# Kernel tuning notes

Hardware: AMD Instinct MI355X
Metric: run time of the kernel (lower is better)

The kernel has to match this reference:

```python
import jax, jax.numpy as jnp
import numpy as np

E = 8        # num_experts
D = 512      # embed_size
H = 8        # attention heads
HD = D // H  # head dim
B, S = 4, 1024


def setup_inputs() -> dict:
    key = jax.random.key(0)
    ks = jax.random.split(key, 16)
    sd = 0.02
    return {
        "x":  jax.random.normal(ks[0], (B, S, D), jnp.float32),
        # per-expert FFN params, stacked over expert dim
        "W1": jax.random.normal(ks[1], (E, D, 4 * D), jnp.float32) * sd,
        "b1": jnp.zeros((E, 4 * D), jnp.float32),
        "W2": jax.random.normal(ks[2], (E, 4 * D, D), jnp.float32) * sd,
        "b2": jnp.zeros((E, D), jnp.float32),
        # MultiheadAttention in_proj (split) and out_proj
        "Wq": jax.random.normal(ks[3], (D, D), jnp.float32) * sd,
        "bq": jnp.zeros((D,), jnp.float32),
        "Wk": jax.random.normal(ks[4], (D, D), jnp.float32) * sd,
        "bk": jnp.zeros((D,), jnp.float32),
        "Wv": jax.random.normal(ks[5], (D, D), jnp.float32) * sd,
        "bv": jnp.zeros((D,), jnp.float32),
        "Wo": jax.random.normal(ks[6], (D, D), jnp.float32) * sd,
        "bo": jnp.zeros((D,), jnp.float32),
        "expert_id": 3,
    }


def reference(x, W1, b1, W2, b2, Wq, bq, Wk, bk, Wv, bv, Wo, bo, expert_id):
    # --- batched per-expert FFN (fuses the Python loop over experts) ---
    # hidden: [B, E, S, 4D]
    hidden = jax.nn.relu(jnp.einsum('bsd,edf->besf', x, W1) + b1[None, :, None, :])
    eo = jnp.einsum('besf,efd->besd', hidden, W2) + b2[None, :, None, :]  # [B,E,S,D]
    eo = eo.transpose(0, 2, 1, 3)  # [B, S, E, D]

    Bs, Ss = x.shape[0], x.shape[1]
    a = eo.reshape(Bs * Ss, E, D)  # [N, E, D]; attention runs over the expert dim

    # --- MultiheadAttention (batch_first), torch semantics ---
    # NOTE: the original passes a FLOAT tril-of-ones attn_mask, which torch ADDS
    # to the scores (it does NOT mask with -inf). We reproduce that faithfully.
    q = (a @ Wq.T + bq).reshape(-1, E, H, HD).transpose(0, 2, 1, 3)  # [N,H,E,hd]
    k = (a @ Wk.T + bk).reshape(-1, E, H, HD).transpose(0, 2, 1, 3)
    v = (a @ Wv.T + bv).reshape(-1, E, H, HD).transpose(0, 2, 1, 3)

    mask = jnp.tril(jnp.ones((E, E), jnp.float32))  # additive float mask
    scores = jnp.einsum('nhed,nhfd->nhef', q, k) / jnp.sqrt(jnp.float32(HD))
    scores = scores + mask[None, None, :, :]
    attn = jax.nn.softmax(scores, axis=-1)
    ctx = jnp.einsum('nhef,nhfd->nhed', attn, v)           # [N,H,E,hd]
    ctx = ctx.transpose(0, 2, 1, 3).reshape(-1, E, D)       # [N,E,D]
    out = ctx @ Wo.T + bo                                   # [N,E,D]

    out = out.reshape(Bs, Ss, E, D)
    return out[:, :, expert_id, :]  # [B, S, D]
```

## Files before the change

### kernel.cpp

```cpp
#include <hip/hip_runtime.h>
#include <hip/hip_bf16.h>

typedef __hip_bfloat16 bf16;
typedef __attribute__((ext_vector_type(4))) float f32x4;
typedef __attribute__((ext_vector_type(8))) short s16x8;

#define N_TOK 4096
#define Dm    512
#define Fm    2048
#define Em    8

__device__ __forceinline__ float bf2f(bf16 v) { return __bfloat162float(v); }
__device__ __forceinline__ bf16  f2bf(float f) { return __float2bfloat16(f); }

#define GL16(g, l)                                                              \
  __builtin_amdgcn_global_load_lds(                                             \
      (const __attribute__((address_space(1))) void*)(g),                       \
      (__attribute__((address_space(3))) void*)(l), 16, 0, 0)

#define BAR()                                   \
  do {                                          \
    __builtin_amdgcn_s_barrier();               \
    asm volatile("" ::: "memory");              \
  } while (0)

__global__ void cvt_f32_bf16(const float* __restrict__ in, bf16* __restrict__ out, int n4) {
  int i = blockIdx.x * 256 + threadIdx.x;
  if (i >= n4) return;
  float4 v = reinterpret_cast<const float4*>(in)[i];
  bf16 tmp[4] = {f2bf(v.x), f2bf(v.y), f2bf(v.z), f2bf(v.w)};
  __builtin_memcpy(out + (size_t)i * 4, tmp, 8);
}

__global__ void transpose_cvt(const float* __restrict__ in, bf16* __restrict__ out,
                              int R, int C, long inb, long outb) {
  in  += (long)blockIdx.z * inb;
  out += (long)blockIdx.z * outb;
  __shared__ float t[32][33];
  int tx = threadIdx.x & 31, ty = threadIdx.x >> 5;
  int c0 = blockIdx.x * 32, r0 = blockIdx.y * 32;
#pragma unroll
  for (int i = 0; i < 32; i += 8)
    t[ty + i][tx] = in[(long)(r0 + ty + i) * C + c0 + tx];
  __syncthreads();
#pragma unroll
  for (int i = 0; i < 32; i += 8)
    out[(long)(c0 + ty + i) * R + r0 + tx] = f2bf(t[tx][ty + i]);
}

template <bool RELU, bool OUT_BF16>
__global__ __launch_bounds__(512, 2) void gemm2b(
    const bf16* __restrict__ A, const bf16* __restrict__ Bt, void* __restrict__ Cout,
    const float* __restrict__ bias, int K, int lda, int ldb, int ldc,
    long abs_, long bbs, long cbs, long biasbs) {
  __shared__ bf16 lds[2 * 16384];

  int e  = blockIdx.z;
  int bm = blockIdx.x * 256, bn = blockIdx.y * 256;

  A    += (long)e * abs_;
  Bt   += (long)e * bbs;
  bias += (long)e * biasbs;
  long coff = (long)e * cbs;

  int tid = threadIdx.x, wv = tid >> 6, lane = tid & 63;
  int wm = wv >> 2, wn = wv & 3;
  int la = lane & 15, q = lane >> 4;

  const bf16* Ab = A + (long)bm * lda;
  const bf16* Bb = Bt + (long)bn * ldb;
  int nt = K >> 5;

  int srow = tid >> 2;
  int ls   = (tid & 3) ^ ((srow >> 1) & 3);
  long aoff0 = (long)srow * lda + ls * 8, aoff1 = aoff0 + (long)128 * lda;
  long boff0 = (long)srow * ldb + ls * 8, boff1 = boff0 + (long)128 * ldb;
  int dst0 = (wv * 64) * 8, dst1 = (512 + wv * 64) * 8;

  auto stage = [&](int t) {
    if (t >= nt) return;
    bf16* buf = lds + (t & 1) * 16384;
    int k0 = t << 5;
    GL16(Ab + aoff0 + k0, buf + dst0);
    GL16(Ab + aoff1 + k0, buf + dst1);
    GL16(Bb + boff0 + k0, buf + 8192 + dst0);
    GL16(Bb + boff1 + k0, buf + 8192 + dst1);
  };

  f32x4 acc[8][4] = {};
  s16x8 af[4], bfr[4];

  stage(0);

  for (int t = 0; t < nt; ++t) {
    asm volatile("s_waitcnt vmcnt(0)" ::: "memory");
    BAR();
    stage(t + 1);
    const bf16* Abuf = lds + (t & 1) * 16384;
    const bf16* Bbuf = Abuf + 8192;
#pragma unroll
    for (int m = 0; m < 4; ++m) {
      int r = wm * 128 + m * 16 + la;
      af[m] = *reinterpret_cast<const s16x8*>(Abuf + r * 32 + ((q ^ ((r >> 1) & 3)) * 8));
    }
#pragma unroll
    for (int n = 0; n < 4; ++n) {
      int r = wn * 64 + n * 16 + la;
      bfr[n] = *reinterpret_cast<const s16x8*>(Bbuf + r * 32 + ((q ^ ((r >> 1) & 3)) * 8));
    }
    __builtin_amdgcn_s_setprio(1);
#pragma unroll
    for (int m = 0; m < 4; ++m)
#pragma unroll
      for (int n = 0; n < 4; ++n)
        acc[m][n] = __builtin_amdgcn_mfma_f32_16x16x32_bf16(bfr[n], af[m], acc[m][n], 0, 0, 0);
    __builtin_amdgcn_s_setprio(0);
#pragma unroll
    for (int m = 0; m < 4; ++m) {
      int r = wm * 128 + 64 + m * 16 + la;
      af[m] = *reinterpret_cast<const s16x8*>(Abuf + r * 32 + ((q ^ ((r >> 1) & 3)) * 8));
    }
    __builtin_amdgcn_s_setprio(1);
#pragma unroll
    for (int m = 0; m < 4; ++m)
#pragma unroll
      for (int n = 0; n < 4; ++n)
        acc[4 + m][n] = __builtin_amdgcn_mfma_f32_16x16x32_bf16(bfr[n], af[m], acc[4 + m][n], 0, 0, 0);
    __builtin_amdgcn_s_setprio(0);
  }

#pragma unroll
  for (int m = 0; m < 8; ++m) {
    int gm = bm + wm * 128 + (m >> 2) * 64 + (m & 3) * 16 + la;
#pragma unroll
    for (int n = 0; n < 4; ++n) {
      int gn = bn + wn * 64 + n * 16 + q * 4;
      float4 b4 = *reinterpret_cast<const float4*>(bias + gn);
      float v0 = acc[m][n][0] + b4.x, v1 = acc[m][n][1] + b4.y;
      float v2 = acc[m][n][2] + b4.z, v3 = acc[m][n][3] + b4.w;
      if (RELU) {
        v0 = fmaxf(v0, 0.f); v1 = fmaxf(v1, 0.f);
        v2 = fmaxf(v2, 0.f); v3 = fmaxf(v3, 0.f);
      }
      long idx = coff + (long)gm * ldc + gn;
      if (OUT_BF16) {
        bf16 tmp[4] = {f2bf(v0), f2bf(v1), f2bf(v2), f2bf(v3)};
        __builtin_memcpy((bf16*)Cout + idx, tmp, 8);
      } else {
        float tmp[4] = {v0, v1, v2, v3};
        __builtin_memcpy((float*)Cout + idx, tmp, 16);
      }
    }
  }
}

template <bool RELU, bool OUT_BF16>
__global__ __launch_bounds__(256, 2) void gemm_bt(
    const bf16* __restrict__ A, const bf16* __restrict__ Bt, void* __restrict__ Cout,
    const float* __restrict__ bias, int M, int N, int K, int lda, int ldb, int ldc,
    long abs_, long bbs, long cbs, long biasbs, const int* __restrict__ eid,
    int eid_scale) {
  int e = blockIdx.z;
  A    += (long)e * abs_;
  Bt   += (long)e * bbs;
  bias += (long)e * biasbs;
  long coff = (long)e * cbs;
  if (eid) A += (long)(*eid) * eid_scale;

  __shared__ bf16 As[128 * 32];
  __shared__ bf16 Bs[128 * 32];

  int tid = threadIdx.x;
  int wave = tid >> 6, lane = tid & 63;
  int wm = wave >> 1, wn = wave & 1;
  int bm = blockIdx.x * 128, bn = blockIdx.y * 128;

  int srow  = lane >> 2;
  int skoff = (lane & 3) * 8;

  f32x4 acc[4][4] = {};

  const bf16* Abase = A + (long)bm * lda;
  const bf16* Bbase = Bt + (long)bn * ldb;

  for (int k0 = 0; k0 < K; k0 += 32) {
    __syncthreads();
#pragma unroll
    for (int i = 0; i < 2; i++) {
      int r = wave * 32 + i * 16 + srow;
      GL16(Abase + (long)r * lda + k0 + skoff, As + (wave * 32 + i * 16) * 32);
      GL16(Bbase + (long)r * ldb + k0 + skoff, Bs + (wave * 32 + i * 16) * 32);
    }
    __syncthreads();

    s16x8 af[4], bfr[4];
#pragma unroll
    for (int m = 0; m < 4; m++)
      af[m] = *reinterpret_cast<const s16x8*>(As + (wm * 64 + m * 16 + (lane & 15)) * 32 +
                                              (lane >> 4) * 8);
#pragma unroll
    for (int n = 0; n < 4; n++)
      bfr[n] = *reinterpret_cast<const s16x8*>(Bs + (wn * 64 + n * 16 + (lane & 15)) * 32 +
                                               (lane >> 4) * 8);
#pragma unroll
    for (int m = 0; m < 4; m++)
#pragma unroll
      for (int n = 0; n < 4; n++)
        acc[m][n] = __builtin_amdgcn_mfma_f32_16x16x32_bf16(af[m], bfr[n], acc[m][n], 0, 0, 0);
  }

  int cr = (lane >> 4) * 4, cc = lane & 15;
#pragma unroll
  for (int m = 0; m < 4; m++) {
#pragma unroll
    for (int n = 0; n < 4; n++) {
      int col  = bn + wn * 64 + n * 16 + cc;
      float bv = bias ? bias[col] : 0.0f;
#pragma unroll
      for (int r = 0; r < 4; r++) {
        int row = bm + wm * 64 + m * 16 + cr + r;
        float v = acc[m][n][r] + bv;
        if (RELU) v = fmaxf(v, 0.0f);
        long idx = coff + (long)row * ldc + col;
        if (OUT_BF16)
          ((bf16*)Cout)[idx] = f2bf(v);
        else
          ((float*)Cout)[idx] = v;
      }
    }
  }
}

__global__ __launch_bounds__(256) void attn_kernel(const float* __restrict__ q,
                                                   const bf16* __restrict__ kv,
                                                   bf16* __restrict__ ctx,
                                                   const int* __restrict__ eid) {
  int wave = threadIdx.x >> 6, lane = threadIdx.x & 63;
  int n = blockIdx.x * 4 + wave;
  int h = lane >> 3, f = lane & 7;
  int e3 = *eid;
  const bf16* kvn = kv + (long)n * Em * (2 * Dm);
  const float* qh = q + (long)n * Dm + h * 64;
  const bf16* kf = kvn + f * (2 * Dm) + h * 64;
  float s = 0.f;
#pragma unroll
  for (int j = 0; j < 64; j++) s += qh[j] * bf2f(kf[j]);
  s *= 0.125f;
  s += (f <= e3) ? 1.0f : 0.0f;
  float mx = s;
#pragma unroll
  for (int d = 1; d < 8; d <<= 1) mx = fmaxf(mx, __shfl_xor(mx, d));
  float ex = expf(s - mx);
  float sm = ex;
#pragma unroll
  for (int d = 1; d < 8; d <<= 1) sm += __shfl_xor(sm, d);
  float at = ex / sm;
  int g = f;
  float acc[8] = {0, 0, 0, 0, 0, 0, 0, 0};
#pragma unroll
  for (int f2 = 0; f2 < 8; f2++) {
    float a = __shfl(at, (h << 3) | f2);
    const bf16* vf = kvn + f2 * (2 * Dm) + Dm + h * 64 + g * 8;
#pragma unroll
    for (int j = 0; j < 8; j++) acc[j] += a * bf2f(vf[j]);
  }
  bf16 tmp[8];
#pragma unroll
  for (int j = 0; j < 8; j++) tmp[j] = f2bf(acc[j]);
  __builtin_memcpy(ctx + (long)n * Dm + h * 64 + g * 8, tmp, 16);
}

extern "C" void kernel_launch(void* const* d_in, const int* in_sizes, int n_in,
                              void* d_out, int out_size, void* d_ws, size_t ws_size,
                              hipStream_t stream) {
  const float* x  = (const float*)d_in[0];
  const float* W1 = (const float*)d_in[1];
  const float* b1 = (const float*)d_in[2];
  const float* W2 = (const float*)d_in[3];
  const float* b2 = (const float*)d_in[4];
  const float* Wq = (const float*)d_in[5];
  const float* bq = (const float*)d_in[6];
  const float* Wk = (const float*)d_in[7];
  const float* bk = (const float*)d_in[8];
  const float* Wv = (const float*)d_in[9];
  const float* bv = (const float*)d_in[10];
  const float* Wo = (const float*)d_in[11];
  const float* bo = (const float*)d_in[12];
  const int* eid  = (const int*)d_in[13];

  char* w = (char*)d_ws;
  auto alloc = [&](size_t bytes) {
    char* p = w;
    w += (bytes + 255) & ~(size_t)255;
    return p;
  };
  bf16* xb   = (bf16*)alloc((size_t)N_TOK * Dm * 2);
  bf16* W1t  = (bf16*)alloc((size_t)Em * Fm * Dm * 2);
  bf16* W2t  = (bf16*)alloc((size_t)Em * Dm * Fm * 2);
  bf16* qw   = (bf16*)alloc((size_t)Dm * Dm * 2);
  bf16* kvw  = (bf16*)alloc((size_t)2 * Dm * Dm * 2);
  bf16* ow   = (bf16*)alloc((size_t)Dm * Dm * 2);
  float* bkv = (float*)alloc((size_t)2 * Dm * 4);
  bf16* hid  = (bf16*)alloc((size_t)Em * N_TOK * Fm * 2);
  bf16* eo   = (bf16*)alloc((size_t)N_TOK * Em * Dm * 2);
  bf16* kv   = (bf16*)hid;
  float* qb  = (float*)(hid + (size_t)N_TOK * Em * 2 * Dm);
  bf16* ctxb = (bf16*)(qb + (size_t)N_TOK * Dm);

  cvt_f32_bf16<<<(N_TOK * Dm / 4 + 255) / 256, 256, 0, stream>>>(x, xb, N_TOK * Dm / 4);
  transpose_cvt<<<dim3(Fm / 32, Dm / 32, Em), 256, 0, stream>>>(
      W1, W1t, Dm, Fm, (long)Dm * Fm, (long)Fm * Dm);
  transpose_cvt<<<dim3(Dm / 32, Fm / 32, Em), 256, 0, stream>>>(
      W2, W2t, Fm, Dm, (long)Fm * Dm, (long)Dm * Fm);
  int nw4 = Dm * Dm / 4;
  cvt_f32_bf16<<<(nw4 + 255) / 256, 256, 0, stream>>>(Wq, qw, nw4);
  cvt_f32_bf16<<<(nw4 + 255) / 256, 256, 0, stream>>>(Wk, kvw, nw4);
  cvt_f32_bf16<<<(nw4 + 255) / 256, 256, 0, stream>>>(Wv, kvw + (size_t)Dm * Dm, nw4);
  cvt_f32_bf16<<<(nw4 + 255) / 256, 256, 0, stream>>>(Wo, ow, nw4);
  hipMemcpyAsync(bkv, bk, Dm * sizeof(float), hipMemcpyDeviceToDevice, stream);
  hipMemcpyAsync(bkv + Dm, bv, Dm * sizeof(float), hipMemcpyDeviceToDevice, stream);

  gemm2b<true, true><<<dim3(16, 8, Em), 512, 0, stream>>>(
      xb, W1t, hid, b1, Dm, Dm, Dm, Fm,
      0L, (long)Fm * Dm, (long)N_TOK * Fm, (long)Fm);
  gemm2b<false, true><<<dim3(16, 2, Em), 512, 0, stream>>>(
      hid, W2t, eo, b2, Fm, Fm, Fm, Em * Dm,
      (long)N_TOK * Fm, (long)Dm * Fm, (long)Dm, (long)Dm);
  gemm2b<false, true><<<dim3(128, 4, 1), 512, 0, stream>>>(
      eo, kvw, kv, bkv, Dm, Dm, Dm, 2 * Dm,
      0L, 0L, 0L, 0L);
  gemm_bt<false, false><<<dim3(N_TOK / 128, Dm / 128, 1), 256, 0, stream>>>(
      eo, qw, qb, bq, N_TOK, Dm, Dm, Em * Dm, Dm, Dm,
      0L, 0L, 0L, 0L, eid, Dm);
  attn_kernel<<<N_TOK / 4, 256, 0, stream>>>(qb, kv, ctxb, eid);
  gemm_bt<false, false><<<dim3(N_TOK / 128, Dm / 128, 1), 256, 0, stream>>>(
      ctxb, ow, (float*)d_out, bo, N_TOK, Dm, Dm, Dm, Dm, Dm,
      0L, 0L, 0L, 0L, nullptr, 0);
}
```

Before: 317.9 us.

## Replace 256x256 LDS GEMM with 128x64 tile loading A directly from global

```diff
diff --git a/kernel.cpp b/kernel.cpp
--- a/kernel.cpp
+++ b/kernel.cpp
@@ -49,46 +49,45 @@
 }
 
 template <bool RELU, bool OUT_BF16>
-__global__ __launch_bounds__(512, 2) void gemm2b(
+__global__ __launch_bounds__(256, 5) void gemm_bs(
     const bf16* __restrict__ A, const bf16* __restrict__ Bt, void* __restrict__ Cout,
     const float* __restrict__ bias, int K, int lda, int ldb, int ldc,
     long abs_, long bbs, long cbs, long biasbs) {
-  __shared__ bf16 lds[2 * 16384];
-
-  int e  = blockIdx.z;
-  int bm = blockIdx.x * 256, bn = blockIdx.y * 256;
-
+  __shared__ bf16 Bs[2][64 * 64];
+
+  int e = blockIdx.z;
   A    += (long)e * abs_;
   Bt   += (long)e * bbs;
   bias += (long)e * biasbs;
   long coff = (long)e * cbs;
 
+  int bm = blockIdx.x * 128, bn = blockIdx.y * 64;
   int tid = threadIdx.x, wv = tid >> 6, lane = tid & 63;
-  int wm = wv >> 2, wn = wv & 3;
   int la = lane & 15, q = lane >> 4;
 
-  const bf16* Ab = A + (long)bm * lda;
   const bf16* Bb = Bt + (long)bn * ldb;
-  int nt = K >> 5;
-
-  int srow = tid >> 2;
-  int ls   = (tid & 3) ^ ((srow >> 1) & 3);
-  long aoff0 = (long)srow * lda + ls * 8, aoff1 = aoff0 + (long)128 * lda;
-  long boff0 = (long)srow * ldb + ls * 8, boff1 = boff0 + (long)128 * ldb;
-  int dst0 = (wv * 64) * 8, dst1 = (512 + wv * 64) * 8;
-
+  int nt = K >> 6;
+
+  int c0 = wv * 128 + lane;
   auto stage = [&](int t) {
     if (t >= nt) return;
-    bf16* buf = lds + (t & 1) * 16384;
-    int k0 = t << 5;
-    GL16(Ab + aoff0 + k0, buf + dst0);
-    GL16(Ab + aoff1 + k0, buf + dst1);
-    GL16(Bb + boff0 + k0, buf + 8192 + dst0);
-    GL16(Bb + boff1 + k0, buf + 8192 + dst1);
+    int k0 = t << 6;
+    bf16* buf = &Bs[t & 1][0];
+#pragma unroll
+    for (int j = 0; j < 2; ++j) {
+      int c   = c0 + j * 64;
+      int row = c >> 3;
+      int src = (c & 7) ^ (row & 7);
+      GL16(Bb + (long)row * ldb + k0 + src * 8, buf + (wv * 128 + j * 64) * 8);
+    }
   };
 
-  f32x4 acc[8][4] = {};
-  s16x8 af[4], bfr[4];
+  const bf16* Ar[2];
+#pragma unroll
+  for (int mi = 0; mi < 2; ++mi)
+    Ar[mi] = A + (long)(bm + wv * 32 + mi * 16 + la) * lda + q * 8;
+
+  f32x4 acc[2][4] = {};
 
   stage(0);
 
@@ -96,48 +95,44 @@
     asm volatile("s_waitcnt vmcnt(0)" ::: "memory");
     BAR();
     stage(t + 1);
-    const bf16* Abuf = lds + (t & 1) * 16384;
-    const bf16* Bbuf = Abuf + 8192;
-#pragma unroll
-    for (int m = 0; m < 4; ++m) {
-      int r = wm * 128 + m * 16 + la;
-      af[m] = *reinterpret_cast<const s16x8*>(Abuf + r * 32 + ((q ^ ((r >> 1) & 3)) * 8));
-    }
+    const bf16* Bbuf = &Bs[t & 1][0];
+    int k0 = t << 6;
+    s16x8 a[2][2], b[4][2];
+#pragma unroll
+    for (int mi = 0; mi < 2; ++mi)
+#pragma unroll
+      for (int kk = 0; kk < 2; ++kk)
+        a[mi][kk] = *reinterpret_cast<const s16x8*>(Ar[mi] + k0 + kk * 32);
 #pragma unroll
     for (int n = 0; n < 4; ++n) {
-      int r = wn * 64 + n * 16 + la;
-      bfr[n] = *reinterpret_cast<const s16x8*>(Bbuf + r * 32 + ((q ^ ((r >> 1) & 3)) * 8));
+      int r = n * 16 + la;
+#pragma unroll
+      for (int kk = 0; kk < 2; ++kk) {
+        int ph = (kk * 4 + q) ^ (r & 7);
+        b[n][kk] = *reinterpret_cast<const s16x8*>(Bbuf + (r * 8 + ph) * 8);
+      }
     }
     __builtin_amdgcn_s_setprio(1);
 #pragma unroll
-    for (int m = 0; m < 4; ++m)
+    for (int mi = 0; mi < 2; ++mi)
 #pragma unroll
       for (int n = 0; n < 4; ++n)
-        acc[m][n] = __builtin_amdgcn_mfma_f32_16x16x32_bf16(bfr[n], af[m], acc[m][n], 0, 0, 0);
+#pragma unroll
+        for (int kk = 0; kk < 2; ++kk)
+          acc[mi][n] = __builtin_amdgcn_mfma_f32_16x16x32_bf16(b[n][kk], a[mi][kk],
+                                                               acc[mi][n], 0, 0, 0);
     __builtin_amdgcn_s_setprio(0);
-#pragma unroll
-    for (int m = 0; m < 4; ++m) {
-      int r = wm * 128 + 64 + m * 16 + la;
-      af[m] = *reinterpret_cast<const s16x8*>(Abuf + r * 32 + ((q ^ ((r >> 1) & 3)) * 8));
-    }
-    __builtin_amdgcn_s_setprio(1);
-#pragma unroll
-    for (int m = 0; m < 4; ++m)
-#pragma unroll
-      for (int n = 0; n < 4; ++n)
-        acc[4 + m][n] = __builtin_amdgcn_mfma_f32_16x16x32_bf16(bfr[n], af[m], acc[4 + m][n], 0, 0, 0);
-    __builtin_amdgcn_s_setprio(0);
-  }
-
-#pragma unroll
-  for (int m = 0; m < 8; ++m) {
-    int gm = bm + wm * 128 + (m >> 2) * 64 + (m & 3) * 16 + la;
+  }
+
+#pragma unroll
+  for (int mi = 0; mi < 2; ++mi) {
+    int gm = bm + wv * 32 + mi * 16 + la;
 #pragma unroll
     for (int n = 0; n < 4; ++n) {
-      int gn = bn + wn * 64 + n * 16 + q * 4;
+      int gn = bn + n * 16 + q * 4;
       float4 b4 = *reinterpret_cast<const float4*>(bias + gn);
-      float v0 = acc[m][n][0] + b4.x, v1 = acc[m][n][1] + b4.y;
-      float v2 = acc[m][n][2] + b4.z, v3 = acc[m][n][3] + b4.w;
+      float v0 = acc[mi][n][0] + b4.x, v1 = acc[mi][n][1] + b4.y;
+      float v2 = acc[mi][n][2] + b4.z, v3 = acc[mi][n][3] + b4.w;
       if (RELU) {
         v0 = fmaxf(v0, 0.f); v1 = fmaxf(v1, 0.f);
         v2 = fmaxf(v2, 0.f); v3 = fmaxf(v3, 0.f);
@@ -320,13 +315,13 @@
   hipMemcpyAsync(bkv, bk, Dm * sizeof(float), hipMemcpyDeviceToDevice, stream);
   hipMemcpyAsync(bkv + Dm, bv, Dm * sizeof(float), hipMemcpyDeviceToDevice, stream);
 
-  gemm2b<true, true><<<dim3(16, 8, Em), 512, 0, stream>>>(
+  gemm_bs<true, true><<<dim3(32, 32, Em), 256, 0, stream>>>(
       xb, W1t, hid, b1, Dm, Dm, Dm, Fm,
       0L, (long)Fm * Dm, (long)N_TOK * Fm, (long)Fm);
-  gemm2b<false, true><<<dim3(16, 2, Em), 512, 0, stream>>>(
+  gemm_bs<false, true><<<dim3(32, 8, Em), 256, 0, stream>>>(
       hid, W2t, eo, b2, Fm, Fm, Fm, Em * Dm,
       (long)N_TOK * Fm, (long)Dm * Fm, (long)Dm, (long)Dm);
-  gemm2b<false, true><<<dim3(128, 4, 1), 512, 0, stream>>>(
+  gemm_bs<false, true><<<dim3(256, 16, 1), 256, 0, stream>>>(
       eo, kvw, kv, bkv, Dm, Dm, Dm, 2 * Dm,
       0L, 0L, 0L, 0L);
   gemm_bt<false, false><<<dim3(N_TOK / 128, Dm / 128, 1), 256, 0, stream>>>(
```

Result: slower. 500.6 us (+57.5%).
